# Kernel tuning notes

Hardware: AMD Instinct MI355X
Metric: run time of the kernel (lower is better)

## Reference

```python
import jax, jax.numpy as jnp
import numpy as np

N = 50000
E = 625000
D_IN = 128
D_OUT = 128


def setup_inputs() -> dict:
    key = jax.random.key(0)
    k1, k2, k3, k4 = jax.random.split(key, 4)
    x = jax.random.normal(k1, (N, D_IN), dtype=jnp.float32)
    edge_index = jax.random.randint(k2, (2, E), 0, N, dtype=jnp.int64)
    edge_weight = jax.random.uniform(k3, (E,), dtype=jnp.float32)
    # xavier_uniform with gain=0.05: limit = gain * sqrt(6/(fan_in+fan_out))
    limit = 0.05 * np.sqrt(6.0 / (D_IN + D_OUT))
    weight = jax.random.uniform(k4, (D_OUT, D_IN), dtype=jnp.float32,
                                minval=-limit, maxval=limit)
    bias = jnp.zeros((D_OUT,), dtype=jnp.float32)
    return {"x": x, "edge_index": edge_index, "edge_weight": edge_weight,
            "weight": weight, "bias": bias}


def reference(x, edge_index, edge_weight, weight, bias):
    src = edge_index[0]
    dst = edge_index[1]
    # gather source features and weight per edge: [E, D_IN]
    msg = x[src] * edge_weight[:, None]
    # scatter-add into destination nodes: [N, D_IN]
    agg = jax.ops.segment_sum(msg, dst, num_segments=x.shape[0])
    # linear + bias + relu
    h = agg @ weight.T + bias
    return jax.nn.relu(h)
```

## Files before the change

### kernel.cpp

```cpp
#include <hip/hip_runtime.h>
#include <hip/hip_fp16.h>

#define NN 50000
#define NE 625000
#define D  128
#define CAP 64
#define NBIN 196
#define BCAP 4096
#define BIN_BLOCKS 200
#define BIN_CHUNK 3125
#define GBM 128
#define PREP_BLKS 3125
#define MEGA_X  BIN_BLOCKS
#define MEGA_W  (BIN_BLOCKS + PREP_BLKS)
#define MEGA_GRID (MEGA_W + 8)

typedef __attribute__((ext_vector_type(8))) short bf16x8;
typedef __attribute__((ext_vector_type(4))) float f32x4;

__device__ inline unsigned f2bf_rne(float f) {
    unsigned u = __float_as_uint(f);
    u += 0x7FFFu + ((u >> 16) & 1u);
    return u >> 16;
}

__device__ inline unsigned pack_hi(float a, float b, float& ra, float& rb) {
    unsigned ba = __float_as_uint(a) & 0xffff0000u;
    unsigned bb = __float_as_uint(b) & 0xffff0000u;
    ra = a - __uint_as_float(ba);
    rb = b - __uint_as_float(bb);
    return (ba >> 16) | bb;
}
__device__ inline unsigned pack_lo(float ra, float rb) {
    return (__float_as_uint(ra) >> 16) | (__float_as_uint(rb) & 0xffff0000u);
}

__global__ __launch_bounds__(256) void mega1(const float* __restrict__ x,
                                             const float* __restrict__ W,
                                             const int* __restrict__ src,
                                             const int* __restrict__ dst,
                                             const float* __restrict__ ew,
                                             unsigned* __restrict__ xb,
                                             ushort* __restrict__ wsp,
                                             int* __restrict__ binc,
                                             uint2* __restrict__ binbuf,
                                             int* __restrict__ ovf_cnt,
                                             uint2* __restrict__ ovf) {
    const int tid = threadIdx.x;
    if (blockIdx.x < MEGA_X) {
        __shared__ int hcnt[4][NBIN];
        __shared__ int hbase[NBIN];
        __shared__ int hcur[NBIN];
        const int wv = tid >> 6;
        const int e0 = blockIdx.x * BIN_CHUNK;
        const int e1 = min(e0 + BIN_CHUNK, NE);
        for (int i = tid; i < NBIN; i += 256) {
            hcnt[0][i] = 0; hcnt[1][i] = 0; hcnt[2][i] = 0; hcnt[3][i] = 0;
        }
        __syncthreads();
        for (int e = e0 + tid; e < e1; e += 256)
            atomicAdd(&hcnt[wv][dst[e] >> 8], 1);
        __syncthreads();
        for (int i = tid; i < NBIN; i += 256) {
            int c = hcnt[0][i] + hcnt[1][i] + hcnt[2][i] + hcnt[3][i];
            hbase[i] = c ? atomicAdd(&binc[i], c) : 0;
            hcur[i] = 0;
        }
        __syncthreads();
        for (int e = e0 + tid; e < e1; e += 256) {
            int d = dst[e];
            int bin = d >> 8;
            unsigned entry = ((unsigned)src[e] << 16) |
                             (unsigned)__half_as_ushort(__float2half(ew[e]));
            int slot = hbase[bin] + atomicAdd(&hcur[bin], 1);
            if (slot < BCAP) {
                binbuf[(size_t)bin * BCAP + slot] = make_uint2((unsigned)d, entry);
            } else {
                int o = atomicAdd(ovf_cnt, 1);
                ovf[o] = make_uint2((unsigned)d, entry);
            }
        }
        return;
    }
    if (blockIdx.x < MEGA_W) {
        int g = (blockIdx.x - MEGA_X) * 256 + tid;
        const float4* xp = (const float4*)(x + (size_t)g * 8);
        float4 a = xp[0], b = xp[1];
        uint4 o;
        o.x = f2bf_rne(a.x) | (f2bf_rne(a.y) << 16);
        o.y = f2bf_rne(a.z) | (f2bf_rne(a.w) << 16);
        o.z = f2bf_rne(b.x) | (f2bf_rne(b.y) << 16);
        o.w = f2bf_rne(b.z) | (f2bf_rne(b.w) << 16);
        ((uint4*)xb)[g] = o;
        return;
    }
    int g = (blockIdx.x - MEGA_W) * 256 + tid;
    if (g >= 128 * 16) return;
    int col = g >> 4;
    int c16 = g & 15;
    const float4* wp = (const float4*)(W + (size_t)col * D + c16 * 8);
    float4 v0 = wp[0], v1 = wp[1];
    float r0, r1, r2, r3, r4, r5, r6, r7;
    uint4 hi, lo;
    hi.x = pack_hi(v0.x, v0.y, r0, r1);
    hi.y = pack_hi(v0.z, v0.w, r2, r3);
    hi.z = pack_hi(v1.x, v1.y, r4, r5);
    hi.w = pack_hi(v1.z, v1.w, r6, r7);
    lo.x = pack_lo(r0, r1); lo.y = pack_lo(r2, r3);
    lo.z = pack_lo(r4, r5); lo.w = pack_lo(r6, r7);
    int sidx = col * 16 + (c16 ^ (col & 15));
    ((uint4*)wsp)[sidx] = hi;
    ((uint4*)(wsp + 16384))[sidx] = lo;
}

__global__ __launch_bounds__(256) void bin_fill(const int* __restrict__ binc,
                                                const uint2* __restrict__ binbuf,
                                                int* __restrict__ fillc,
                                                unsigned* __restrict__ buck,
                                                int* __restrict__ ovf_cnt,
                                                uint2* __restrict__ ovf) {
    __shared__ int lcnt[256];
    const int tid = threadIdx.x;
    const int bin = blockIdx.x;
    lcnt[tid] = 0;
    __syncthreads();
    int n = binc[bin];
    if (n > BCAP) n = BCAP;
    const uint2* bp = binbuf + (size_t)bin * BCAP;
    for (int i = tid; i < n; i += 256) {
        uint2 q = bp[i];
        int d = (int)q.x;
        int p = atomicAdd(&lcnt[d & 255], 1);
        if (p < CAP) {
            buck[(size_t)d * CAP + p] = q.y;
        } else {
            int o = atomicAdd(ovf_cnt, 1);
            ovf[o] = q;
        }
    }
    __syncthreads();
    int node = bin * 256 + tid;
    if (node < NN) fillc[node] = lcnt[tid];
}

__global__ __launch_bounds__(256) void aggregate(const unsigned* __restrict__ xb,
                                                 const int* __restrict__ fillc,
                                                 const unsigned* __restrict__ buck,
                                                 const int* __restrict__ ovf_cnt,
                                                 const uint2* __restrict__ ovf,
                                                 float* __restrict__ agg) {
    const int node = blockIdx.x * 8 + ((threadIdx.x >> 5));
    const int t = threadIdx.x & 31;
    int cnt = fillc[node];
    if (cnt > CAP) cnt = CAP;
    const unsigned* bp = buck + (size_t)node * CAP;
    const uint2* x2 = (const uint2*)xb;
    float4 acc = {0.f, 0.f, 0.f, 0.f};
    int i = 0;
    for (; i + 3 < cnt; i += 4) {
        unsigned q0 = bp[i], q1 = bp[i + 1], q2 = bp[i + 2], q3 = bp[i + 3];
        uint2 u0 = x2[(size_t)(q0 >> 16) * 32 + t];
        uint2 u1 = x2[(size_t)(q1 >> 16) * 32 + t];
        uint2 u2 = x2[(size_t)(q2 >> 16) * 32 + t];
        uint2 u3 = x2[(size_t)(q3 >> 16) * 32 + t];
        float w0 = __half2float(__ushort_as_half((ushort)(q0 & 0xffffu)));
        float w1 = __half2float(__ushort_as_half((ushort)(q1 & 0xffffu)));
        float w2 = __half2float(__ushort_as_half((ushort)(q2 & 0xffffu)));
        float w3 = __half2float(__ushort_as_half((ushort)(q3 & 0xffffu)));
        acc.x += __uint_as_float(u0.x << 16) * w0;
        acc.y += __uint_as_float(u0.x & 0xffff0000u) * w0;
        acc.z += __uint_as_float(u0.y << 16) * w0;
        acc.w += __uint_as_float(u0.y & 0xffff0000u) * w0;
        acc.x += __uint_as_float(u1.x << 16) * w1;
        acc.y += __uint_as_float(u1.x & 0xffff0000u) * w1;
        acc.z += __uint_as_float(u1.y << 16) * w1;
        acc.w += __uint_as_float(u1.y & 0xffff0000u) * w1;
        acc.x += __uint_as_float(u2.x << 16) * w2;
        acc.y += __uint_as_float(u2.x & 0xffff0000u) * w2;
        acc.z += __uint_as_float(u2.y << 16) * w2;
        acc.w += __uint_as_float(u2.y & 0xffff0000u) * w2;
        acc.x += __uint_as_float(u3.x << 16) * w3;
        acc.y += __uint_as_float(u3.x & 0xffff0000u) * w3;
        acc.z += __uint_as_float(u3.y << 16) * w3;
        acc.w += __uint_as_float(u3.y & 0xffff0000u) * w3;
    }
    for (; i < cnt; ++i) {
        unsigned q0 = bp[i];
        uint2 u0 = x2[(size_t)(q0 >> 16) * 32 + t];
        float w0 = __half2float(__ushort_as_half((ushort)(q0 & 0xffffu)));
        acc.x += __uint_as_float(u0.x << 16) * w0;
        acc.y += __uint_as_float(u0.x & 0xffff0000u) * w0;
        acc.z += __uint_as_float(u0.y << 16) * w0;
        acc.w += __uint_as_float(u0.y & 0xffff0000u) * w0;
    }
    int n = *ovf_cnt;
    for (int o = 0; o < n; ++o) {
        uint2 q = ovf[o];
        if ((int)q.x == node) {
            uint2 u = x2[(size_t)(q.y >> 16) * 32 + t];
            float w = __half2float(__ushort_as_half((ushort)(q.y & 0xffffu)));
            acc.x += __uint_as_float(u.x << 16) * w;
            acc.y += __uint_as_float(u.x & 0xffff0000u) * w;
            acc.z += __uint_as_float(u.y << 16) * w;
            acc.w += __uint_as_float(u.y & 0xffff0000u) * w;
        }
    }
    ((float4*)agg)[(size_t)node * 32 + t] = acc;
}

__global__ __launch_bounds__(256) void gemm_mfma(const float* __restrict__ agg,
                                                 const ushort* __restrict__ wsp,
                                                 const float* __restrict__ bias,
                                                 float* __restrict__ out) {
    __shared__ ushort wl[32768];
    const int tid = threadIdx.x;
    {
        const uint4* s = (const uint4*)wsp;
        uint4* d = (uint4*)wl;
#pragma unroll
        for (int i = 0; i < 16; ++i)
            d[i * 256 + tid] = s[i * 256 + tid];
    }
    __syncthreads();

    const int wid = tid >> 6, lane = tid & 63;
    const int l15 = lane & 15, kg = lane >> 4;
    const int wrbase = blockIdx.x * GBM + wid * 32;

    f32x4 acc[2][8];
    const f32x4 fz = {0.f, 0.f, 0.f, 0.f};
#pragma unroll
    for (int m = 0; m < 2; ++m)
#pragma unroll
        for (int n = 0; n < 8; ++n) acc[m][n] = fz;

    int arow0 = wrbase + l15;
    int arow1 = wrbase + 16 + l15;
    const float* a0p = agg + (size_t)(arow0 < NN ? arow0 : NN - 1) * D + kg * 8;
    const float* a1p = agg + (size_t)(arow1 < NN ? arow1 : NN - 1) * D + kg * 8;

#pragma unroll
    for (int kk = 0; kk < 4; ++kk) {
        float4 u0 = *(const float4*)(a0p + kk * 32);
        float4 u1 = *(const float4*)(a0p + kk * 32 + 4);
        float4 v0 = *(const float4*)(a1p + kk * 32);
        float4 v1 = *(const float4*)(a1p + kk * 32 + 4);
        float r0, r1, r2, r3, r4, r5, r6, r7;
        uint4 h0, l0, h1, l1;
        h0.x = pack_hi(u0.x, u0.y, r0, r1);
        h0.y = pack_hi(u0.z, u0.w, r2, r3);
        h0.z = pack_hi(u1.x, u1.y, r4, r5);
        h0.w = pack_hi(u1.z, u1.w, r6, r7);
        l0.x = pack_lo(r0, r1); l0.y = pack_lo(r2, r3);
        l0.z = pack_lo(r4, r5); l0.w = pack_lo(r6, r7);
        h1.x = pack_hi(v0.x, v0.y, r0, r1);
        h1.y = pack_hi(v0.z, v0.w, r2, r3);
        h1.z = pack_hi(v1.x, v1.y, r4, r5);
        h1.w = pack_hi(v1.z, v1.w, r6, r7);
        l1.x = pack_lo(r0, r1); l1.y = pack_lo(r2, r3);
        l1.z = pack_lo(r4, r5); l1.w = pack_lo(r6, r7);
        bf16x8 a0hi = *(bf16x8*)&h0;
        bf16x8 a0lo = *(bf16x8*)&l0;
        bf16x8 a1hi = *(bf16x8*)&h1;
        bf16x8 a1lo = *(bf16x8*)&l1;

        int coff = ((kk * 4 + kg) ^ l15) * 8;
#pragma unroll
        for (int nf = 0; nf < 8; ++nf) {
            int bidx = (16 * nf + l15) * 128 + coff;
            bf16x8 bhi = *(const bf16x8*)&wl[bidx];
            bf16x8 blo = *(const bf16x8*)&wl[16384 + bidx];
            acc[0][nf] = __builtin_amdgcn_mfma_f32_16x16x32_bf16(a0hi, bhi, acc[0][nf], 0, 0, 0);
            acc[1][nf] = __builtin_amdgcn_mfma_f32_16x16x32_bf16(a1hi, bhi, acc[1][nf], 0, 0, 0);
            acc[0][nf] = __builtin_amdgcn_mfma_f32_16x16x32_bf16(a0lo, bhi, acc[0][nf], 0, 0, 0);
            acc[1][nf] = __builtin_amdgcn_mfma_f32_16x16x32_bf16(a1lo, bhi, acc[1][nf], 0, 0, 0);
            acc[0][nf] = __builtin_amdgcn_mfma_f32_16x16x32_bf16(a0hi, blo, acc[0][nf], 0, 0, 0);
            acc[1][nf] = __builtin_amdgcn_mfma_f32_16x16x32_bf16(a1hi, blo, acc[1][nf], 0, 0, 0);
        }
    }

    const int rofs = kg * 4;
#pragma unroll
    for (int nf = 0; nf < 8; ++nf) {
        int col = 16 * nf + l15;
        float bv = bias[col];
#pragma unroll
        for (int m = 0; m < 2; ++m) {
#pragma unroll
            for (int r = 0; r < 4; ++r) {
                int row = wrbase + 16 * m + rofs + r;
                if (row < NN) {
                    float h = acc[m][nf][r] + bv;
                    out[(size_t)row * D + col] = h > 0.f ? h : 0.f;
                }
            }
        }
    }
}

extern "C" void kernel_launch(void* const* d_in, const int* in_sizes, int n_in,
                              void* d_out, int out_size, void* d_ws, size_t ws_size,
                              hipStream_t stream) {
    const float* x    = (const float*)d_in[0];
    const int*   eidx = (const int*)d_in[1];
    const float* ew   = (const float*)d_in[2];
    const float* W    = (const float*)d_in[3];
    const float* bias = (const float*)d_in[4];
    float* out = (float*)d_out;

    const int* src = eidx;
    const int* dst = eidx + NE;

    char* base = (char*)d_ws;
    float*    agg    = (float*)base;
    uint2*    binbuf = (uint2*)base;
    unsigned* buck   = (unsigned*)(base + 25600000);
    unsigned* xb     = (unsigned*)(base + 25600000 + 12800000);
    ushort*   wsp    = (ushort*)(base + 51200000);
    int*      fillc   = (int*)(base + 51200000 + 65536);
    int*      binc    = (int*)(base + 51200000 + 65536 + 200000);
    int*      ovf_cnt = (int*)((char*)binc + NBIN * 4);
    uint2*    ovf     = (uint2*)(base + 51200000 + 65536 + 200000 + 1024);

    hipMemsetAsync(binc, 0, NBIN * 4 + 4, stream);
    mega1<<<MEGA_GRID, 256, 0, stream>>>(x, W, src, dst, ew, xb, wsp, binc, binbuf, ovf_cnt, ovf);
    bin_fill<<<NBIN, 256, 0, stream>>>(binc, binbuf, fillc, buck, ovf_cnt, ovf);
    aggregate<<<6250, 256, 0, stream>>>(xb, fillc, buck, ovf_cnt, ovf, agg);
    gemm_mfma<<<(NN + GBM - 1) / GBM, 256, 0, stream>>>(agg, wsp, bias, out);
}
```

Before: 85.50 us.

## Store aggregates as bf16, drop lo-split MFMAs, pad buckets for vector loads

The aggregate kernel now rounds its fp32 accumulators to bf16 and writes half-size output. The GEMM then loads the bf16 rows directly instead of splitting fp32 into hi/lo bf16 pairs, which cuts MFMA count from six to four per fragment. Bucket lists are zero-padded to a multiple of four so aggregate can read four entries with one uint4 load and skip the scalar tail loop. This trades accuracy on the aggregated activations for less memory traffic and compute, and adds small padding writes in bin_fill.

```diff
diff --git a/kernel.cpp b/kernel.cpp
--- a/kernel.cpp
+++ b/kernel.cpp
@@ -140,7 +140,14 @@
     }
     __syncthreads();
     int node = bin * 256 + tid;
-    if (node < NN) fillc[node] = lcnt[tid];
+    if (node < NN) {
+        int c = lcnt[tid];
+        if (c > CAP) c = CAP;
+        int pc = (c + 3) & ~3;
+        for (int p = c; p < pc; ++p)
+            buck[(size_t)node * CAP + p] = 0;
+        fillc[node] = pc;
+    }
 }
 
 __global__ __launch_bounds__(256) void aggregate(const unsigned* __restrict__ xb,
@@ -148,25 +155,25 @@
                                                  const unsigned* __restrict__ buck,
                                                  const int* __restrict__ ovf_cnt,
                                                  const uint2* __restrict__ ovf,
-                                                 float* __restrict__ agg) {
-    const int node = blockIdx.x * 8 + ((threadIdx.x >> 5));
+                                                 unsigned* __restrict__ aggb) {
+    const int node = blockIdx.x * 8 + (threadIdx.x >> 5);
     const int t = threadIdx.x & 31;
     int cnt = fillc[node];
     if (cnt > CAP) cnt = CAP;
-    const unsigned* bp = buck + (size_t)node * CAP;
+    const uint4* bp4 = (const uint4*)(buck + (size_t)node * CAP);
     const uint2* x2 = (const uint2*)xb;
     float4 acc = {0.f, 0.f, 0.f, 0.f};
-    int i = 0;
-    for (; i + 3 < cnt; i += 4) {
-        unsigned q0 = bp[i], q1 = bp[i + 1], q2 = bp[i + 2], q3 = bp[i + 3];
-        uint2 u0 = x2[(size_t)(q0 >> 16) * 32 + t];
-        uint2 u1 = x2[(size_t)(q1 >> 16) * 32 + t];
-        uint2 u2 = x2[(size_t)(q2 >> 16) * 32 + t];
-        uint2 u3 = x2[(size_t)(q3 >> 16) * 32 + t];
-        float w0 = __half2float(__ushort_as_half((ushort)(q0 & 0xffffu)));
-        float w1 = __half2float(__ushort_as_half((ushort)(q1 & 0xffffu)));
-        float w2 = __half2float(__ushort_as_half((ushort)(q2 & 0xffffu)));
-        float w3 = __half2float(__ushort_as_half((ushort)(q3 & 0xffffu)));
+    int n4 = cnt >> 2;
+    for (int i = 0; i < n4; ++i) {
+        uint4 q = bp4[i];
+        uint2 u0 = x2[(size_t)(q.x >> 16) * 32 + t];
+        uint2 u1 = x2[(size_t)(q.y >> 16) * 32 + t];
+        uint2 u2 = x2[(size_t)(q.z >> 16) * 32 + t];
+        uint2 u3 = x2[(size_t)(q.w >> 16) * 32 + t];
+        float w0 = __half2float(__ushort_as_half((ushort)(q.x & 0xffffu)));
+        float w1 = __half2float(__ushort_as_half((ushort)(q.y & 0xffffu)));
+        float w2 = __half2float(__ushort_as_half((ushort)(q.z & 0xffffu)));
+        float w3 = __half2float(__ushort_as_half((ushort)(q.w & 0xffffu)));
         acc.x += __uint_as_float(u0.x << 16) * w0;
         acc.y += __uint_as_float(u0.x & 0xffff0000u) * w0;
         acc.z += __uint_as_float(u0.y << 16) * w0;
@@ -184,15 +191,6 @@
         acc.z += __uint_as_float(u3.y << 16) * w3;
         acc.w += __uint_as_float(u3.y & 0xffff0000u) * w3;
     }
-    for (; i < cnt; ++i) {
-        unsigned q0 = bp[i];
-        uint2 u0 = x2[(size_t)(q0 >> 16) * 32 + t];
-        float w0 = __half2float(__ushort_as_half((ushort)(q0 & 0xffffu)));
-        acc.x += __uint_as_float(u0.x << 16) * w0;
-        acc.y += __uint_as_float(u0.x & 0xffff0000u) * w0;
-        acc.z += __uint_as_float(u0.y << 16) * w0;
-        acc.w += __uint_as_float(u0.y & 0xffff0000u) * w0;
-    }
     int n = *ovf_cnt;
     for (int o = 0; o < n; ++o) {
         uint2 q = ovf[o];
@@ -205,10 +203,12 @@
             acc.w += __uint_as_float(u.y & 0xffff0000u) * w;
         }
     }
-    ((float4*)agg)[(size_t)node * 32 + t] = acc;
-}
-
-__global__ __launch_bounds__(256) void gemm_mfma(const float* __restrict__ agg,
+    unsigned o0 = f2bf_rne(acc.x) | (f2bf_rne(acc.y) << 16);
+    unsigned o1 = f2bf_rne(acc.z) | (f2bf_rne(acc.w) << 16);
+    ((uint2*)aggb)[(size_t)node * 32 + t] = make_uint2(o0, o1);
+}
+
+__global__ __launch_bounds__(256) void gemm_mfma(const unsigned* __restrict__ aggb,
                                                  const ushort* __restrict__ wsp,
                                                  const float* __restrict__ bias,
                                                  float* __restrict__ out) {
@@ -236,33 +236,15 @@
 
     int arow0 = wrbase + l15;
     int arow1 = wrbase + 16 + l15;
-    const float* a0p = agg + (size_t)(arow0 < NN ? arow0 : NN - 1) * D + kg * 8;
-    const float* a1p = agg + (size_t)(arow1 < NN ? arow1 : NN - 1) * D + kg * 8;
+    const unsigned* a0p = aggb + (size_t)(arow0 < NN ? arow0 : NN - 1) * 64 + kg * 4;
+    const unsigned* a1p = aggb + (size_t)(arow1 < NN ? arow1 : NN - 1) * 64 + kg * 4;
 
 #pragma unroll
     for (int kk = 0; kk < 4; ++kk) {
-        float4 u0 = *(const float4*)(a0p + kk * 32);
-        float4 u1 = *(const float4*)(a0p + kk * 32 + 4);
-        float4 v0 = *(const float4*)(a1p + kk * 32);
-        float4 v1 = *(const float4*)(a1p + kk * 32 + 4);
-        float r0, r1, r2, r3, r4, r5, r6, r7;
-        uint4 h0, l0, h1, l1;
-        h0.x = pack_hi(u0.x, u0.y, r0, r1);
-        h0.y = pack_hi(u0.z, u0.w, r2, r3);
-        h0.z = pack_hi(u1.x, u1.y, r4, r5);
-        h0.w = pack_hi(u1.z, u1.w, r6, r7);
-        l0.x = pack_lo(r0, r1); l0.y = pack_lo(r2, r3);
-        l0.z = pack_lo(r4, r5); l0.w = pack_lo(r6, r7);
-        h1.x = pack_hi(v0.x, v0.y, r0, r1);
-        h1.y = pack_hi(v0.z, v0.w, r2, r3);
-        h1.z = pack_hi(v1.x, v1.y, r4, r5);
-        h1.w = pack_hi(v1.z, v1.w, r6, r7);
-        l1.x = pack_lo(r0, r1); l1.y = pack_lo(r2, r3);
-        l1.z = pack_lo(r4, r5); l1.w = pack_lo(r6, r7);
-        bf16x8 a0hi = *(bf16x8*)&h0;
-        bf16x8 a0lo = *(bf16x8*)&l0;
-        bf16x8 a1hi = *(bf16x8*)&h1;
-        bf16x8 a1lo = *(bf16x8*)&l1;
+        uint4 h0 = *(const uint4*)(a0p + kk * 16);
+        uint4 h1 = *(const uint4*)(a1p + kk * 16);
+        bf16x8 a0 = *(bf16x8*)&h0;
+        bf16x8 a1 = *(bf16x8*)&h1;
 
         int coff = ((kk * 4 + kg) ^ l15) * 8;
 #pragma unroll
@@ -270,12 +252,10 @@
             int bidx = (16 * nf + l15) * 128 + coff;
             bf16x8 bhi = *(const bf16x8*)&wl[bidx];
             bf16x8 blo = *(const bf16x8*)&wl[16384 + bidx];
-            acc[0][nf] = __builtin_amdgcn_mfma_f32_16x16x32_bf16(a0hi, bhi, acc[0][nf], 0, 0, 0);
-            acc[1][nf] = __builtin_amdgcn_mfma_f32_16x16x32_bf16(a1hi, bhi, acc[1][nf], 0, 0, 0);
-            acc[0][nf] = __builtin_amdgcn_mfma_f32_16x16x32_bf16(a0lo, bhi, acc[0][nf], 0, 0, 0);
-            acc[1][nf] = __builtin_amdgcn_mfma_f32_16x16x32_bf16(a1lo, bhi, acc[1][nf], 0, 0, 0);
-            acc[0][nf] = __builtin_amdgcn_mfma_f32_16x16x32_bf16(a0hi, blo, acc[0][nf], 0, 0, 0);
-            acc[1][nf] = __builtin_amdgcn_mfma_f32_16x16x32_bf16(a1hi, blo, acc[1][nf], 0, 0, 0);
+            acc[0][nf] = __builtin_amdgcn_mfma_f32_16x16x32_bf16(a0, bhi, acc[0][nf], 0, 0, 0);
+            acc[1][nf] = __builtin_amdgcn_mfma_f32_16x16x32_bf16(a1, bhi, acc[1][nf], 0, 0, 0);
+            acc[0][nf] = __builtin_amdgcn_mfma_f32_16x16x32_bf16(a0, blo, acc[0][nf], 0, 0, 0);
+            acc[1][nf] = __builtin_amdgcn_mfma_f32_16x16x32_bf16(a1, blo, acc[1][nf], 0, 0, 0);
         }
     }
 
@@ -312,7 +292,7 @@
     const int* dst = eidx + NE;
 
     char* base = (char*)d_ws;
-    float*    agg    = (float*)base;
+    unsigned* aggb   = (unsigned*)base;
     uint2*    binbuf = (uint2*)base;
     unsigned* buck   = (unsigned*)(base + 25600000);
     unsigned* xb     = (unsigned*)(base + 25600000 + 12800000);
@@ -325,6 +305,6 @@
     hipMemsetAsync(binc, 0, NBIN * 4 + 4, stream);
     mega1<<<MEGA_GRID, 256, 0, stream>>>(x, W, src, dst, ew, xb, wsp, binc, binbuf, ovf_cnt, ovf);
     bin_fill<<<NBIN, 256, 0, stream>>>(binc, binbuf, fillc, buck, ovf_cnt, ovf);
-    aggregate<<<6250, 256, 0, stream>>>(xb, fillc, buck, ovf_cnt, ovf, agg);
-    gemm_mfma<<<(NN + GBM - 1) / GBM, 256, 0, stream>>>(agg, wsp, bias, out);
-}
+    aggregate<<<6250, 256, 0, stream>>>(xb, fillc, buck, ovf_cnt, ovf, aggb);
+    gemm_mfma<<<(NN + GBM - 1) / GBM, 256, 0, stream>>>(aggb, wsp, bias, out);
+}
```

After: 79.72 us (median of 2 runs). 1.07x faster.
